# Kernel optimization log

Measured on AMD Instinct MI355X. Metric: run time of the kernel, lower is better.

## Reference

```python
import jax, jax.numpy as jnp
import numpy as np
import math

EMBED = 512
KDIM = 512
VDIM = 512
H = 8
HD = EMBED // H
N = 2048
L = 2048
B = 4


def setup_inputs() -> dict:
    key = jax.random.key(0)
    ks = jax.random.split(key, 14)
    s = 1.0 / math.sqrt(EMBED)
    return {
        "q": jax.random.normal(ks[0], (N, B, EMBED), jnp.float32),
        "k": jax.random.normal(ks[1], (L, B, KDIM), jnp.float32),
        "v": jax.random.normal(ks[2], (L, B, VDIM), jnp.float32),
        "pe1": jax.random.normal(ks[3], (B, N, 3), jnp.float32),
        "pe2": jax.random.normal(ks[4], (L, 3), jnp.float32),
        "Wq": jax.random.normal(ks[5], (EMBED, EMBED), jnp.float32) * s,
        "bq": jnp.zeros((EMBED,), jnp.float32),
        "Wk": jax.random.normal(ks[6], (EMBED, KDIM), jnp.float32) * s,
        "bk": jnp.zeros((EMBED,), jnp.float32),
        "Wv": jax.random.normal(ks[7], (EMBED, VDIM), jnp.float32) * s,
        "bv": jnp.zeros((EMBED,), jnp.float32),
        "Wo": jax.random.normal(ks[8], (EMBED, EMBED), jnp.float32) * s,
        "bo": jnp.zeros((EMBED,), jnp.float32),
    }


def reference(q, k, v, pe1, pe2, Wq, bq, Wk, bk, Wv, bv, Wo, bo):
    n, b, _ = q.shape
    l = k.shape[0]
    # projections (nn.Linear: x @ W.T + b)
    qp = q @ Wq.T + bq  # (n, b, E)
    kp = k @ Wk.T + bk  # (l, b, E)
    vp = v @ Wv.T + bv  # (l, b, E)
    # split heads -> (b, H, n, hd)
    qh = qp.reshape(n, b, H, HD).transpose(1, 2, 0, 3)
    kh = kp.reshape(l, b, H, HD).transpose(1, 2, 0, 3)
    vh = vp.reshape(l, b, H, HD).transpose(1, 2, 0, 3)
    # relative PE bias: (b, n, l), broadcast over heads
    pe_scores = jnp.einsum('bnc,lc->bnl', pe1, pe2)[:, None, :, :]
    scores = (jnp.einsum('bhnd,bhld->bhnl', qh, kh) + pe_scores) / math.sqrt(HD)
    attn = jax.nn.softmax(scores, axis=-1)
    out = jnp.einsum('bhnl,bhld->bhnd', attn, vh)  # (b, H, n, hd)
    out = out.transpose(2, 0, 1, 3).reshape(n, b, EMBED)
    return out @ Wo.T + bo
```

## Files before the change

### kernel.cpp

```cpp
#include <hip/hip_runtime.h>
#include <math.h>

#define EMBED 512
#define HDIM 64
#define NHEADS 8
#define SEQ_N 2048
#define SEQ_L 2048
#define BATCH 4
#define MROWS (SEQ_N*BATCH)
#define BE (BATCH*EMBED)

#define QSCALE 0.18033688f

typedef _Float16 f16;
typedef _Float16 half8 __attribute__((ext_vector_type(8)));
typedef _Float16 half4 __attribute__((ext_vector_type(4)));
typedef _Float16 half2v __attribute__((ext_vector_type(2)));
typedef float floatx4 __attribute__((ext_vector_type(4)));
typedef float floatx16 __attribute__((ext_vector_type(16)));

static __device__ inline float fast_exp2(float x) {
#if __has_builtin(__builtin_amdgcn_exp2f)
  return __builtin_amdgcn_exp2f(x);
#else
  return __expf(x * 0.69314718056f);
#endif
}

static __device__ inline half2v pk2(float a, float b) {
#if __has_builtin(__builtin_amdgcn_cvt_pkrtz)
  return __builtin_bit_cast(half2v, __builtin_amdgcn_cvt_pkrtz(a, b));
#else
  half2v o; o[0] = (f16)a; o[1] = (f16)b; return o;
#endif
}

static __device__ inline half8 cvt8(const float4& a, const float4& b) {
  half2v p0 = pk2(a.x, a.y), p1 = pk2(a.z, a.w);
  half2v p2 = pk2(b.x, b.y), p3 = pk2(b.z, b.w);
  half8 o;
  o[0] = p0[0]; o[1] = p0[1]; o[2] = p1[0]; o[3] = p1[1];
  o[4] = p2[0]; o[5] = p2[1]; o[6] = p3[0]; o[7] = p3[1];
  return o;
}

__global__ __launch_bounds__(256) void gemm_qkv(const float* __restrict__ A0,
                                                const float* __restrict__ A1,
                                                const float* __restrict__ A2,
                                                const float* __restrict__ W0,
                                                const float* __restrict__ W1,
                                                const float* __restrict__ W2,
                                                const float* __restrict__ b0,
                                                const float* __restrict__ b1,
                                                const float* __restrict__ b2,
                                                f16* __restrict__ C0, f16* __restrict__ C1,
                                                f16* __restrict__ C2t) {
  __shared__ alignas(16) f16 As[128 * 40];
  __shared__ alignas(16) f16 Bs[128 * 40];
  const int sel = blockIdx.y >> 2;
  const float* A = sel == 0 ? A0 : sel == 1 ? A1 : A2;
  const float* Bt = sel == 0 ? W0 : sel == 1 ? W1 : W2;
  const float* bias = sel == 0 ? b0 : sel == 1 ? b1 : b2;
  const float scl = sel == 0 ? QSCALE : 1.0f;
  const int tid = threadIdx.x;
  const int wave = tid >> 6, lane = tid & 63, quad = lane >> 4, l16 = lane & 15;
  const int wm = wave & 1, wn = wave >> 1;
  const long m0 = (long)blockIdx.x * 128;
  const long n0 = (long)(blockIdx.y & 3) * 128;
  floatx4 acc[4][4] = {};
  const int r0 = tid >> 2;
  const int c0 = (tid & 3) * 8;

  for (int k0 = 0; k0 < EMBED; k0 += 32) {
    __syncthreads();
    float4 a00 = *reinterpret_cast<const float4*>(A + (m0 + r0) * EMBED + k0 + c0);
    float4 a01 = *reinterpret_cast<const float4*>(A + (m0 + r0) * EMBED + k0 + c0 + 4);
    float4 a10 = *reinterpret_cast<const float4*>(A + (m0 + r0 + 64) * EMBED + k0 + c0);
    float4 a11 = *reinterpret_cast<const float4*>(A + (m0 + r0 + 64) * EMBED + k0 + c0 + 4);
    float4 w00 = *reinterpret_cast<const float4*>(Bt + (n0 + r0) * EMBED + k0 + c0);
    float4 w01 = *reinterpret_cast<const float4*>(Bt + (n0 + r0) * EMBED + k0 + c0 + 4);
    float4 w10 = *reinterpret_cast<const float4*>(Bt + (n0 + r0 + 64) * EMBED + k0 + c0);
    float4 w11 = *reinterpret_cast<const float4*>(Bt + (n0 + r0 + 64) * EMBED + k0 + c0 + 4);
    *reinterpret_cast<half8*>(&As[r0 * 40 + c0]) = cvt8(a00, a01);
    *reinterpret_cast<half8*>(&As[(r0 + 64) * 40 + c0]) = cvt8(a10, a11);
    *reinterpret_cast<half8*>(&Bs[r0 * 40 + c0]) = cvt8(w00, w01);
    *reinterpret_cast<half8*>(&Bs[(r0 + 64) * 40 + c0]) = cvt8(w10, w11);
    __syncthreads();
    half8 af[4], bf[4];
#pragma unroll
    for (int i = 0; i < 4; ++i)
      af[i] = *reinterpret_cast<const half8*>(&As[(wm * 64 + i * 16 + l16) * 40 + quad * 8]);
#pragma unroll
    for (int j = 0; j < 4; ++j)
      bf[j] = *reinterpret_cast<const half8*>(&Bs[(wn * 64 + j * 16 + l16) * 40 + quad * 8]);
#pragma unroll
    for (int i = 0; i < 4; ++i)
#pragma unroll
      for (int j = 0; j < 4; ++j)
        acc[i][j] = __builtin_amdgcn_mfma_f32_16x16x32_f16(af[i], bf[j], acc[i][j], 0, 0, 0);
  }
#pragma unroll
  for (int i = 0; i < 4; ++i)
#pragma unroll
    for (int r = 0; r < 4; ++r) {
      long row = m0 + wm * 64 + i * 16 + quad * 4 + r;
#pragma unroll
      for (int j = 0; j < 4; ++j) {
        long col = n0 + wn * 64 + j * 16 + l16;
        float val = (acc[i][j][r] + bias[col]) * scl;
        if (sel == 2) {
          long bq = row & 3, ltok = row >> 2;
          long hh = col >> 6, dd = col & 63;
          C2t[(((bq << 3) + hh) * 64 + dd) * 2048 + ltok] = (f16)val;
        } else {
          f16* C = sel == 0 ? C0 : C1;
          C[row * EMBED + col] = (f16)val;
        }
      }
    }
}

__global__ __launch_bounds__(256) void gemm_out(const f16* __restrict__ A,
                                                const float* __restrict__ Wt,
                                                const float* __restrict__ bias,
                                                float* __restrict__ C) {
  __shared__ alignas(16) f16 As[128 * 40];
  __shared__ alignas(16) f16 Bs[64 * 40];
  const int tid = threadIdx.x;
  const int wave = tid >> 6, lane = tid & 63, quad = lane >> 4, l16 = lane & 15;
  const long m0 = (long)blockIdx.x * 128;
  const long n0 = (long)blockIdx.y * 64;
  floatx4 acc[2][4] = {};
  const int r0 = tid >> 2;
  const int c0 = (tid & 3) * 8;

  for (int k0 = 0; k0 < EMBED; k0 += 32) {
    __syncthreads();
    uint4 a0 = *reinterpret_cast<const uint4*>(A + (m0 + r0) * EMBED + k0 + c0);
    uint4 a1 = *reinterpret_cast<const uint4*>(A + (m0 + r0 + 64) * EMBED + k0 + c0);
    float4 w0 = *reinterpret_cast<const float4*>(Wt + (n0 + r0) * EMBED + k0 + c0);
    float4 w1 = *reinterpret_cast<const float4*>(Wt + (n0 + r0) * EMBED + k0 + c0 + 4);
    *reinterpret_cast<uint4*>(&As[r0 * 40 + c0]) = a0;
    *reinterpret_cast<uint4*>(&As[(r0 + 64) * 40 + c0]) = a1;
    *reinterpret_cast<half8*>(&Bs[r0 * 40 + c0]) = cvt8(w0, w1);
    __syncthreads();
    half8 af[2], bf[4];
#pragma unroll
    for (int i = 0; i < 2; ++i)
      af[i] = *reinterpret_cast<const half8*>(&As[(wave * 32 + i * 16 + l16) * 40 + quad * 8]);
#pragma unroll
    for (int j = 0; j < 4; ++j)
      bf[j] = *reinterpret_cast<const half8*>(&Bs[(j * 16 + l16) * 40 + quad * 8]);
#pragma unroll
    for (int i = 0; i < 2; ++i)
#pragma unroll
      for (int j = 0; j < 4; ++j)
        acc[i][j] = __builtin_amdgcn_mfma_f32_16x16x32_f16(af[i], bf[j], acc[i][j], 0, 0, 0);
  }
#pragma unroll
  for (int i = 0; i < 2; ++i)
#pragma unroll
    for (int r = 0; r < 4; ++r) {
      long row = m0 + wave * 32 + i * 16 + quad * 4 + r;
#pragma unroll
      for (int j = 0; j < 4; ++j) {
        long col = n0 + j * 16 + l16;
        C[row * EMBED + col] = acc[i][j][r] + bias[col];
      }
    }
}

#define KST 88
#define VST 136
#define NCHUNK (SEQ_L / 128)
#define LDSB (128 * KST * 2 + 64 * VST * 2)
__global__ __launch_bounds__(512, 4) void attn_flash(const f16* __restrict__ qp,
                                                     const f16* __restrict__ kp,
                                                     const f16* __restrict__ vt,
                                                     const float* __restrict__ pe1,
                                                     const float* __restrict__ pe2,
                                                     f16* __restrict__ ao) {
  __shared__ alignas(16) unsigned char smem[LDSB];
  f16* Ks = reinterpret_cast<f16*>(smem);
  f16* Vt = reinterpret_cast<f16*>(smem + 128 * KST * 2);
  float* comb = reinterpret_cast<float*>(smem);
  const int tid = threadIdx.x, wave = tid >> 6, lane = tid & 63;
  const int m = lane & 31, h = lane >> 5;
  const int strip = wave & 3, half = wave >> 2;
  const int n0 = blockIdx.x * 128;
  const int b = blockIdx.y >> 3, hd = blockIdx.y & 7;
  const long headoff = (long)b * EMBED + hd * HDIM;
  const long vhead = (long)blockIdx.y * 64 * 2048;

  for (int c = tid; c < 1024; c += 512) {
    int r = c >> 3, col = (c & 7) * 8;
    *reinterpret_cast<uint4*>(&Ks[r * KST + col]) =
        *reinterpret_cast<const uint4*>(qp + (long)(n0 + r) * BE + headoff + col);
    int rv = c >> 4, cv = (c & 15) * 8;
    *reinterpret_cast<uint4*>(&Vt[rv * VST + cv]) =
        *reinterpret_cast<const uint4*>(vt + vhead + (long)rv * 2048 + 0 + cv);
  }
  {
    const uint4 z4 = {0, 0, 0, 0};
    const uint2 z2 = {0, 0};
    int r = tid >> 2, s = tid & 3;
    if (s == 0) *reinterpret_cast<uint2*>(&Ks[r * KST + 68]) = z2;
    else if (s == 1) *reinterpret_cast<uint4*>(&Ks[r * KST + 72]) = z4;
    else if (s == 2) *reinterpret_cast<uint4*>(&Ks[r * KST + 80]) = z4;
  }
  if (tid < 128) {
    long base = ((long)b * SEQ_N + n0 + tid) * 3;
    half4 v8;
    v8[0] = (f16)(pe1[base + 0] * QSCALE);
    v8[1] = (f16)(pe1[base + 1] * QSCALE);
    v8[2] = (f16)(pe1[base + 2] * QSCALE);
    v8[3] = (f16)0.f;
    *reinterpret_cast<half4*>(&Ks[tid * KST + 64]) = v8;
  }
  __syncthreads();

  half8 qf[5];
#pragma unroll
  for (int e = 0; e < 5; ++e)
    qf[e] = *reinterpret_cast<const half8*>(&Ks[(strip * 32 + m) * KST + e * 16 + h * 8]);
  __syncthreads();

  for (int c = tid; c < 1024; c += 512) {
    int r = c >> 3, col = (c & 7) * 8;
    *reinterpret_cast<uint4*>(&Ks[r * KST + col]) =
        *reinterpret_cast<const uint4*>(kp + (long)(0 + r) * BE + headoff + col);
  }
  if (tid < 128) {
    long bb = (long)(0 + tid) * 3;
    half4 p2;
    p2[0] = (f16)pe2[bb + 0]; p2[1] = (f16)pe2[bb + 1];
    p2[2] = (f16)pe2[bb + 2]; p2[3] = (f16)0.f;
    *reinterpret_cast<half4*>(&Ks[tid * KST + 64]) = p2;
  }

  floatx16 oacc[2] = {};
  float lpart = 0.f;

#pragma unroll 1
  for (int c = 0; c < NCHUNK; ++c) {
    __syncthreads();
#pragma unroll
    for (int tt = 0; tt < 2; ++tt) {
      const int t = half * 2 + tt;
      floatx16 st = {};
#pragma unroll
      for (int e = 0; e < 5; ++e) {
        half8 kf = *reinterpret_cast<const half8*>(&Ks[(t * 32 + m) * KST + e * 16 + h * 8]);
        st = __builtin_amdgcn_mfma_f32_32x32x16_f16(kf, qf[e], st, 0, 0, 0);
      }
      float p[16];
#pragma unroll
      for (int r = 0; r < 16; ++r) {
        p[r] = fast_exp2(st[r]);
        lpart += p[r];
      }
#pragma unroll
      for (int s = 0; s < 4; ++s) {
        half2v u0 = pk2(p[4 * s + 0], p[4 * s + 1]);
        half2v u1 = pk2(p[4 * s + 2], p[4 * s + 3]);
        half4 bp;
        bp[0] = u0[0]; bp[1] = u0[1]; bp[2] = u1[0]; bp[3] = u1[1];
        int lcol = t * 32 + s * 8 + h * 4;
#pragma unroll
        for (int dt = 0; dt < 2; ++dt) {
          half4 vf = *reinterpret_cast<const half4*>(&Vt[(dt * 32 + m) * VST + lcol]);
          oacc[dt] = __builtin_amdgcn_mfma_f32_32x32x8f16(vf, bp, oacc[dt], 0, 0, 0);
        }
      }
    }
    __syncthreads();
    if (c + 1 < NCHUNK) {
      const int l0 = (c + 1) * 128;
      for (int cc = tid; cc < 1024; cc += 512) {
        int r = cc >> 3, col = (cc & 7) * 8;
        *reinterpret_cast<uint4*>(&Ks[r * KST + col]) =
            *reinterpret_cast<const uint4*>(kp + (long)(l0 + r) * BE + headoff + col);
        int rv = cc >> 4, cv = (cc & 15) * 8;
        *reinterpret_cast<uint4*>(&Vt[rv * VST + cv]) =
            *reinterpret_cast<const uint4*>(vt + vhead + (long)rv * 2048 + l0 + cv);
      }
      if (tid < 128) {
        long bb = (long)(l0 + tid) * 3;
        half4 p2;
        p2[0] = (f16)pe2[bb + 0]; p2[1] = (f16)pe2[bb + 1];
        p2[2] = (f16)pe2[bb + 2]; p2[3] = (f16)0.f;
        *reinterpret_cast<half4*>(&Ks[tid * KST + 64]) = p2;
      }
    }
  }

  lpart += __shfl_xor(lpart, 32);

  if (half == 1) {
    float* dst = comb + (strip * 64 + lane) * 33;
#pragma unroll
    for (int dt = 0; dt < 2; ++dt)
#pragma unroll
      for (int x = 0; x < 16; ++x) dst[dt * 16 + x] = oacc[dt][x];
    dst[32] = lpart;
  }
  __syncthreads();
  if (half == 0) {
    const float* src = comb + (strip * 64 + lane) * 33;
#pragma unroll
    for (int dt = 0; dt < 2; ++dt)
#pragma unroll
      for (int x = 0; x < 16; ++x) oacc[dt][x] += src[dt * 16 + x];
    float inv = 1.f / (lpart + src[32]);
    long qrow = n0 + strip * 32 + m;
#pragma unroll
    for (int dt = 0; dt < 2; ++dt)
#pragma unroll
      for (int g = 0; g < 4; ++g) {
        half4 o4;
#pragma unroll
        for (int x = 0; x < 4; ++x) o4[x] = (f16)(oacc[dt][4 * g + x] * inv);
        int d = dt * 32 + 8 * g + 4 * h;
        *reinterpret_cast<half4*>(ao + qrow * BE + headoff + d) = o4;
      }
  }
}

extern "C" void kernel_launch(void* const* d_in, const int* in_sizes, int n_in,
                              void* d_out, int out_size, void* d_ws, size_t ws_size,
                              hipStream_t stream) {
  const float* q   = (const float*)d_in[0];
  const float* k   = (const float*)d_in[1];
  const float* v   = (const float*)d_in[2];
  const float* pe1 = (const float*)d_in[3];
  const float* pe2 = (const float*)d_in[4];
  const float* Wq  = (const float*)d_in[5];
  const float* bq  = (const float*)d_in[6];
  const float* Wk  = (const float*)d_in[7];
  const float* bk  = (const float*)d_in[8];
  const float* Wv  = (const float*)d_in[9];
  const float* bv  = (const float*)d_in[10];
  const float* Wo  = (const float*)d_in[11];
  const float* bo  = (const float*)d_in[12];
  float* out = (float*)d_out;

  f16* ws = (f16*)d_ws;
  const long TOK = (long)MROWS * EMBED;
  f16* qpb = ws;
  f16* kpb = qpb + TOK;
  f16* vtb = kpb + TOK;
  f16* aob = vtb + TOK;

  gemm_qkv<<<dim3(MROWS / 128, 12), 256, 0, stream>>>(q, k, v, Wq, Wk, Wv,
                                                      bq, bk, bv, qpb, kpb, vtb);

  attn_flash<<<dim3(SEQ_N / 128, BATCH * NHEADS), 512, 0, stream>>>(qpb, kpb, vtb, pe1, pe2, aob);

  gemm_out<<<dim3(MROWS / 128, EMBED / 64), 256, 0, stream>>>(aob, Wo, bo, out);
}
```

Before: 212.8 us.

## Pre-convert inputs and weights to fp16, stage GEMM tiles via global_load_lds

Adds a separate conversion kernel that casts q, k, v and all four weight matrices to fp16 in workspace, then rewrites both projection GEMMs to load fp16 tiles straight into LDS with the global_load_lds builtin. This removes the per-tile float-to-half conversion and the register round trip in the GEMM inner loops. In exchange it adds an extra launch and a full extra read and write pass over the fp32 activations. The LDS padding is also dropped from 40 to 32 halves per row, which may bring back bank conflicts on the fragment reads.

```diff
diff --git a/kernel.cpp b/kernel.cpp
--- a/kernel.cpp
+++ b/kernel.cpp
@@ -35,31 +35,61 @@
 #endif
 }
 
-static __device__ inline half8 cvt8(const float4& a, const float4& b) {
-  half2v p0 = pk2(a.x, a.y), p1 = pk2(a.z, a.w);
-  half2v p2 = pk2(b.x, b.y), p3 = pk2(b.z, b.w);
-  half8 o;
-  o[0] = p0[0]; o[1] = p0[1]; o[2] = p1[0]; o[3] = p1[1];
-  o[4] = p2[0]; o[5] = p2[1]; o[6] = p3[0]; o[7] = p3[1];
-  return o;
-}
-
-__global__ __launch_bounds__(256) void gemm_qkv(const float* __restrict__ A0,
-                                                const float* __restrict__ A1,
-                                                const float* __restrict__ A2,
-                                                const float* __restrict__ W0,
-                                                const float* __restrict__ W1,
-                                                const float* __restrict__ W2,
+static __device__ inline void gload16(const void* g, void* l) {
+  __builtin_amdgcn_global_load_lds(
+      (__attribute__((address_space(1))) void*)(g),
+      (__attribute__((address_space(3))) void*)(l), 16, 0, 0);
+}
+
+__global__ __launch_bounds__(256) void cvt_all(const float* __restrict__ q,
+                                               const float* __restrict__ k,
+                                               const float* __restrict__ v,
+                                               const float* __restrict__ Wq,
+                                               const float* __restrict__ Wk,
+                                               const float* __restrict__ Wv,
+                                               const float* __restrict__ Wo,
+                                               f16* __restrict__ qb, f16* __restrict__ kb,
+                                               f16* __restrict__ vb, f16* __restrict__ Wb) {
+  const long TOK = (long)MROWS * EMBED;
+  const long WSZ = (long)EMBED * EMBED;
+  int y = blockIdx.y;
+  long i = ((long)blockIdx.x * 256 + threadIdx.x) * 4;
+  if (y < 3) {
+    if (i < TOK) {
+      const float* s = y == 0 ? q : y == 1 ? k : v;
+      f16* d = y == 0 ? qb : y == 1 ? kb : vb;
+      float4 f = *reinterpret_cast<const float4*>(s + i);
+      half4 o; o[0] = (f16)f.x; o[1] = (f16)f.y; o[2] = (f16)f.z; o[3] = (f16)f.w;
+      *reinterpret_cast<half4*>(d + i) = o;
+    }
+  } else {
+    if (i < 4 * WSZ) {
+      int sel = (int)(i >> 18);
+      long off = i & (WSZ - 1);
+      const float* s = sel == 0 ? Wq : sel == 1 ? Wk : sel == 2 ? Wv : Wo;
+      float4 f = *reinterpret_cast<const float4*>(s + off);
+      half4 o; o[0] = (f16)f.x; o[1] = (f16)f.y; o[2] = (f16)f.z; o[3] = (f16)f.w;
+      *reinterpret_cast<half4*>(Wb + i) = o;
+    }
+  }
+}
+
+__global__ __launch_bounds__(256) void gemm_qkv(const f16* __restrict__ A0,
+                                                const f16* __restrict__ A1,
+                                                const f16* __restrict__ A2,
+                                                const f16* __restrict__ W0,
+                                                const f16* __restrict__ W1,
+                                                const f16* __restrict__ W2,
                                                 const float* __restrict__ b0,
                                                 const float* __restrict__ b1,
                                                 const float* __restrict__ b2,
                                                 f16* __restrict__ C0, f16* __restrict__ C1,
                                                 f16* __restrict__ C2t) {
-  __shared__ alignas(16) f16 As[128 * 40];
-  __shared__ alignas(16) f16 Bs[128 * 40];
+  __shared__ alignas(16) f16 As[128 * 32];
+  __shared__ alignas(16) f16 Bs[128 * 32];
   const int sel = blockIdx.y >> 2;
-  const float* A = sel == 0 ? A0 : sel == 1 ? A1 : A2;
-  const float* Bt = sel == 0 ? W0 : sel == 1 ? W1 : W2;
+  const f16* A = sel == 0 ? A0 : sel == 1 ? A1 : A2;
+  const f16* Bt = sel == 0 ? W0 : sel == 1 ? W1 : W2;
   const float* bias = sel == 0 ? b0 : sel == 1 ? b1 : b2;
   const float scl = sel == 0 ? QSCALE : 1.0f;
   const int tid = threadIdx.x;
@@ -68,31 +98,23 @@
   const long m0 = (long)blockIdx.x * 128;
   const long n0 = (long)(blockIdx.y & 3) * 128;
   floatx4 acc[4][4] = {};
-  const int r0 = tid >> 2;
-  const int c0 = (tid & 3) * 8;
+  const int srow = lane >> 2;
+  const int scol = (lane & 3) * 8;
 
   for (int k0 = 0; k0 < EMBED; k0 += 32) {
     __syncthreads();
-    float4 a00 = *reinterpret_cast<const float4*>(A + (m0 + r0) * EMBED + k0 + c0);
-    float4 a01 = *reinterpret_cast<const float4*>(A + (m0 + r0) * EMBED + k0 + c0 + 4);
-    float4 a10 = *reinterpret_cast<const float4*>(A + (m0 + r0 + 64) * EMBED + k0 + c0);
-    float4 a11 = *reinterpret_cast<const float4*>(A + (m0 + r0 + 64) * EMBED + k0 + c0 + 4);
-    float4 w00 = *reinterpret_cast<const float4*>(Bt + (n0 + r0) * EMBED + k0 + c0);
-    float4 w01 = *reinterpret_cast<const float4*>(Bt + (n0 + r0) * EMBED + k0 + c0 + 4);
-    float4 w10 = *reinterpret_cast<const float4*>(Bt + (n0 + r0 + 64) * EMBED + k0 + c0);
-    float4 w11 = *reinterpret_cast<const float4*>(Bt + (n0 + r0 + 64) * EMBED + k0 + c0 + 4);
-    *reinterpret_cast<half8*>(&As[r0 * 40 + c0]) = cvt8(a00, a01);
-    *reinterpret_cast<half8*>(&As[(r0 + 64) * 40 + c0]) = cvt8(a10, a11);
-    *reinterpret_cast<half8*>(&Bs[r0 * 40 + c0]) = cvt8(w00, w01);
-    *reinterpret_cast<half8*>(&Bs[(r0 + 64) * 40 + c0]) = cvt8(w10, w11);
+    gload16(A + (m0 + wave * 32 + srow) * EMBED + k0 + scol, &As[(wave * 32) * 32]);
+    gload16(A + (m0 + wave * 32 + 16 + srow) * EMBED + k0 + scol, &As[(wave * 32 + 16) * 32]);
+    gload16(Bt + (n0 + wave * 32 + srow) * EMBED + k0 + scol, &Bs[(wave * 32) * 32]);
+    gload16(Bt + (n0 + wave * 32 + 16 + srow) * EMBED + k0 + scol, &Bs[(wave * 32 + 16) * 32]);
     __syncthreads();
     half8 af[4], bf[4];
 #pragma unroll
     for (int i = 0; i < 4; ++i)
-      af[i] = *reinterpret_cast<const half8*>(&As[(wm * 64 + i * 16 + l16) * 40 + quad * 8]);
+      af[i] = *reinterpret_cast<const half8*>(&As[(wm * 64 + i * 16 + l16) * 32 + quad * 8]);
 #pragma unroll
     for (int j = 0; j < 4; ++j)
-      bf[j] = *reinterpret_cast<const half8*>(&Bs[(wn * 64 + j * 16 + l16) * 40 + quad * 8]);
+      bf[j] = *reinterpret_cast<const half8*>(&Bs[(wn * 64 + j * 16 + l16) * 32 + quad * 8]);
 #pragma unroll
     for (int i = 0; i < 4; ++i)
 #pragma unroll
@@ -121,36 +143,32 @@
 }
 
 __global__ __launch_bounds__(256) void gemm_out(const f16* __restrict__ A,
-                                                const float* __restrict__ Wt,
+                                                const f16* __restrict__ Bt,
                                                 const float* __restrict__ bias,
                                                 float* __restrict__ C) {
-  __shared__ alignas(16) f16 As[128 * 40];
-  __shared__ alignas(16) f16 Bs[64 * 40];
+  __shared__ alignas(16) f16 As[128 * 32];
+  __shared__ alignas(16) f16 Bs[64 * 32];
   const int tid = threadIdx.x;
   const int wave = tid >> 6, lane = tid & 63, quad = lane >> 4, l16 = lane & 15;
   const long m0 = (long)blockIdx.x * 128;
   const long n0 = (long)blockIdx.y * 64;
   floatx4 acc[2][4] = {};
-  const int r0 = tid >> 2;
-  const int c0 = (tid & 3) * 8;
+  const int srow = lane >> 2;
+  const int scol = (lane & 3) * 8;
 
   for (int k0 = 0; k0 < EMBED; k0 += 32) {
     __syncthreads();
-    uint4 a0 = *reinterpret_cast<const uint4*>(A + (m0 + r0) * EMBED + k0 + c0);
-    uint4 a1 = *reinterpret_cast<const uint4*>(A + (m0 + r0 + 64) * EMBED + k0 + c0);
-    float4 w0 = *reinterpret_cast<const float4*>(Wt + (n0 + r0) * EMBED + k0 + c0);
-    float4 w1 = *reinterpret_cast<const float4*>(Wt + (n0 + r0) * EMBED + k0 + c0 + 4);
-    *reinterpret_cast<uint4*>(&As[r0 * 40 + c0]) = a0;
-    *reinterpret_cast<uint4*>(&As[(r0 + 64) * 40 + c0]) = a1;
-    *reinterpret_cast<half8*>(&Bs[r0 * 40 + c0]) = cvt8(w0, w1);
+    gload16(A + (m0 + wave * 32 + srow) * EMBED + k0 + scol, &As[(wave * 32) * 32]);
+    gload16(A + (m0 + wave * 32 + 16 + srow) * EMBED + k0 + scol, &As[(wave * 32 + 16) * 32]);
+    gload16(Bt + (n0 + wave * 16 + srow) * EMBED + k0 + scol, &Bs[(wave * 16) * 32]);
     __syncthreads();
     half8 af[2], bf[4];
 #pragma unroll
     for (int i = 0; i < 2; ++i)
-      af[i] = *reinterpret_cast<const half8*>(&As[(wave * 32 + i * 16 + l16) * 40 + quad * 8]);
+      af[i] = *reinterpret_cast<const half8*>(&As[(wave * 32 + i * 16 + l16) * 32 + quad * 8]);
 #pragma unroll
     for (int j = 0; j < 4; ++j)
-      bf[j] = *reinterpret_cast<const half8*>(&Bs[(j * 16 + l16) * 40 + quad * 8]);
+      bf[j] = *reinterpret_cast<const half8*>(&Bs[(j * 16 + l16) * 32 + quad * 8]);
 #pragma unroll
     for (int i = 0; i < 2; ++i)
 #pragma unroll
@@ -346,15 +364,25 @@
 
   f16* ws = (f16*)d_ws;
   const long TOK = (long)MROWS * EMBED;
-  f16* qpb = ws;
+  const long WSZ = (long)EMBED * EMBED;
+  f16* qb  = ws;
+  f16* kb  = qb + TOK;
+  f16* vb  = kb + TOK;
+  f16* Wqb = vb + TOK;
+  f16* Wkb = Wqb + WSZ;
+  f16* Wvb = Wkb + WSZ;
+  f16* Wob = Wvb + WSZ;
+  f16* qpb = Wob + WSZ;
   f16* kpb = qpb + TOK;
   f16* vtb = kpb + TOK;
   f16* aob = vtb + TOK;
 
-  gemm_qkv<<<dim3(MROWS / 128, 12), 256, 0, stream>>>(q, k, v, Wq, Wk, Wv,
+  cvt_all<<<dim3(4096, 4), 256, 0, stream>>>(q, k, v, Wq, Wk, Wv, Wo, qb, kb, vb, Wqb);
+
+  gemm_qkv<<<dim3(MROWS / 128, 12), 256, 0, stream>>>(qb, kb, vb, Wqb, Wkb, Wvb,
                                                       bq, bk, bv, qpb, kpb, vtb);
 
   attn_flash<<<dim3(SEQ_N / 128, BATCH * NHEADS), 512, 0, stream>>>(qpb, kpb, vtb, pe1, pe2, aob);
 
-  gemm_out<<<dim3(MROWS / 128, EMBED / 64), 256, 0, stream>>>(aob, Wo, bo, out);
-}
+  gemm_out<<<dim3(MROWS / 128, EMBED / 64), 256, 0, stream>>>(aob, Wob, bo, out);
+}
```

Measured after the change: 203.9 us. 1.04x faster.
